# Performance work log

Hardware: AMD Instinct MI355X
Metric: run time of the kernel (lower is better)

The kernel has to match this reference:

```python
import jax, jax.numpy as jnp
import numpy as np

WS = 7        # window size (cubic)
SHIFT = 3     # shift size (cubic)
NH = 6        # num heads
EPS = 1e-5


def _layernorm(x, g, b):
    m = x.mean(-1, keepdims=True)
    v = ((x - m) ** 2).mean(-1, keepdims=True)
    return (x - m) / jnp.sqrt(v + EPS) * g + b


def _win_partition(x, ws):
    # (B,H,W,T,C) -> (B*nW, ws^3, C)
    B, H, W, T, C = x.shape
    x = x.reshape(B, H // ws, ws, W // ws, ws, T // ws, ws, C)
    return x.transpose(0, 1, 3, 5, 2, 4, 6, 7).reshape(-1, ws * ws * ws, C)


def _win_reverse(w, ws, B, H, W, T):
    # (B*nW, ws^3, C) -> (B,H,W,T,C)
    C = w.shape[-1]
    x = w.reshape(B, H // ws, W // ws, T // ws, ws, ws, ws, C)
    return x.transpose(0, 1, 4, 2, 5, 3, 6, 7).reshape(B, H, W, T, C)


def _rel_index(ws):
    # 3D relative position index, (N, N) int, N = ws^3 (torch.meshgrid default 'ij')
    coords = np.stack(np.meshgrid(np.arange(ws), np.arange(ws), np.arange(ws), indexing='ij'))
    cf = coords.reshape(3, -1)
    rel = (cf[:, :, None] - cf[:, None, :]).transpose(1, 2, 0)
    rel[:, :, 0] += ws - 1
    rel[:, :, 1] += ws - 1
    rel[:, :, 2] += ws - 1
    rel[:, :, 0] *= (2 * ws - 1) ** 2
    rel[:, :, 1] *= (2 * ws - 1)
    return rel.sum(-1)


def _compute_mask(Hp, Wp, Tp, ws, shift):
    img = np.zeros((1, Hp, Wp, Tp, 1), np.float32)
    cnt = 0
    sl = (slice(0, -ws), slice(-ws, -shift), slice(-shift, None))
    for h in sl:
        for w in sl:
            for t in sl:
                img[:, h, w, t, :] = cnt
                cnt += 1
    mw = np.asarray(_win_partition(jnp.asarray(img), ws)).reshape(-1, ws ** 3)  # (nW, N)
    am = mw[:, None, :] - mw[:, :, None]
    return jnp.asarray(np.where(am != 0, -100.0, 0.0).astype(np.float32))


def setup_inputs() -> dict:
    key = jax.random.key(0)
    ks = jax.random.split(key, 10)
    B, Hd, Wd, Td, C = 2, 28, 28, 28, 192
    L = Hd * Wd * Td
    Ch = int(C * 4.0)
    s = 0.02
    inp = {
        'x': jax.random.normal(ks[0], (B, L, C), jnp.float32),
        'mask': _compute_mask(Hd, Wd, Td, WS, SHIFT),
        'gamma1': jnp.ones((C,), jnp.float32),
        'beta1': jnp.zeros((C,), jnp.float32),
        'qkv_w': jax.random.normal(ks[1], (3 * C, C), jnp.float32) * s,
        'qkv_b': jnp.zeros((3 * C,), jnp.float32),
        'rpb_table': jax.random.normal(ks[2], ((2 * WS - 1) ** 3, NH), jnp.float32) * s,
        'proj_w': jax.random.normal(ks[3], (C, C), jnp.float32) * s,
        'proj_b': jnp.zeros((C,), jnp.float32),
        'gamma2': jnp.ones((C,), jnp.float32),
        'beta2': jnp.zeros((C,), jnp.float32),
        'fc1_w': jax.random.normal(ks[4], (Ch, C), jnp.float32) * s,
        'fc1_b': jnp.zeros((Ch,), jnp.float32),
        'fc2_w': jax.random.normal(ks[5], (C, Ch), jnp.float32) * s,
        'fc2_b': jnp.zeros((C,), jnp.float32),
        'H': Hd, 'W': Wd, 'T': Td,
    }
    return inp


def reference(x, mask, gamma1, beta1, qkv_w, qkv_b, rpb_table, proj_w, proj_b,
              gamma2, beta2, fc1_w, fc1_b, fc2_w, fc2_b, H, W, T):
    B, L, C = x.shape
    hd = C // NH
    scale = hd ** -0.5
    shortcut = x

    h1 = _layernorm(x, gamma1, beta1).reshape(B, H, W, T, C)
    # H,W,T are multiples of WS -> no padding; cyclic shift for SW-MSA
    shifted = jnp.roll(h1, (-SHIFT, -SHIFT, -SHIFT), axis=(1, 2, 3))
    xw = _win_partition(shifted, WS)            # (B*nW, N, C)
    Bn, N, _ = xw.shape

    qkv = (xw @ qkv_w.T + qkv_b).reshape(Bn, N, 3, NH, hd).transpose(2, 0, 3, 1, 4)
    q, k, v = qkv[0] * scale, qkv[1], qkv[2]     # (Bn, NH, N, hd)
    attn = jnp.einsum('bhnd,bhmd->bhnm', q, k)   # (Bn, NH, N, N)

    idx = _rel_index(WS)
    bias = rpb_table[idx.reshape(-1)].reshape(N, N, NH).transpose(2, 0, 1)
    attn = attn + bias[None]

    nW = mask.shape[0]
    attn = attn.reshape(Bn // nW, nW, NH, N, N) + mask[None, :, None]
    attn = jax.nn.softmax(attn.reshape(Bn, NH, N, N), axis=-1)

    out = jnp.einsum('bhnm,bhmd->bhnd', attn, v).transpose(0, 2, 1, 3).reshape(Bn, N, C)
    out = out @ proj_w.T + proj_b

    shifted = _win_reverse(out, WS, B, H, W, T)
    xr = jnp.roll(shifted, (SHIFT, SHIFT, SHIFT), axis=(1, 2, 3)).reshape(B, L, C)

    x = shortcut + xr
    h2 = _layernorm(x, gamma2, beta2)
    m = jax.nn.gelu(h2 @ fc1_w.T + fc1_b, approximate=False)
    return x + (m @ fc2_w.T + fc2_b)
```

## Files before the change

kernel.cpp:

```cpp
#include <hip/hip_runtime.h>
#include <hip/hip_bf16.h>

typedef unsigned short u16;
typedef unsigned int u32;
typedef __attribute__((ext_vector_type(8))) short s16x8;
typedef __attribute__((ext_vector_type(4))) float f32x4;

__device__ __forceinline__ float bf2f(u16 v) {
    union { u32 u; float f; } x; x.u = ((u32)v) << 16; return x.f;
}
__device__ __forceinline__ u16 f2bf(float f) {
    union { float f; u32 u; } x; x.f = f;
    u32 r = x.u + 0x7fffu + ((x.u >> 16) & 1u);
    return (u16)(r >> 16);
}

#define L_TOK 21952
#define C_DIM 192
#define ATT_SCALE 0.17677669529663687f

__global__ __launch_bounds__(256) void cvt_k(const float* __restrict__ s0,
                                             const float* __restrict__ s1,
                                             const float* __restrict__ s2,
                                             const float* __restrict__ s3,
                                             u16* __restrict__ dst)
{
    int i = blockIdx.x * 256 + threadIdx.x;
    float v;
    if (i < 110592) v = s0[i];
    else if (i < 147456) v = s1[i - 110592];
    else if (i < 294912) v = s2[i - 147456];
    else v = s3[i - 294912];
    dst[i] = f2bf(v);
}

__global__ __launch_bounds__(256) void bias6_k(const float* __restrict__ rpb,
                                               u16* __restrict__ bias6)
{
    const int m = blockIdx.x * 256 + threadIdx.x;
    if (m >= 343) return;
    const int n = blockIdx.y, hh = blockIdx.z;
    int hq = n / 49, r1 = n - hq * 49, wq = r1 / 7, tq = r1 - wq * 7;
    int hm = m / 49, r2 = m - hm * 49, wm = r2 / 7, tm = r2 - wm * 7;
    int idx = ((hq - hm + 6) * 13 + (wq - wm + 6)) * 13 + (tq - tm + 6);
    bias6[((size_t)hh * 343 + n) * 343 + m] = f2bf(rpb[idx * 6 + hh]);
}

template<int MODE>
__global__ __launch_bounds__(256) void ln_k(const float* __restrict__ in,
                                            const float* __restrict__ g,
                                            const float* __restrict__ b,
                                            u16* __restrict__ out)
{
    const int lane = threadIdx.x & 63, wv = threadIdx.x >> 6;
    const int tok = blockIdx.x * 4 + wv;
    size_t base = (size_t)tok * C_DIM;
    float x0 = in[base + lane];
    float x1 = in[base + 64 + lane];
    float x2 = in[base + 128 + lane];
    float s = x0 + x1 + x2;
    float sq = x0 * x0 + x1 * x1 + x2 * x2;
    #pragma unroll
    for (int off = 32; off > 0; off >>= 1) {
        s += __shfl_xor(s, off, 64);
        sq += __shfl_xor(sq, off, 64);
    }
    const float mean = s * (1.0f / 192.0f);
    float var = sq * (1.0f / 192.0f) - mean * mean;
    var = fmaxf(var, 0.0f);
    const float rstd = rsqrtf(var + 1e-5f);

    size_t obase;
    if (MODE == 0) {
        int bi = tok / L_TOK;
        int l = tok - bi * L_TOK;
        int h = l / 784;
        int rm = l - h * 784;
        int w = rm / 28;
        int t = rm - w * 28;
        int hs = h + 25; if (hs >= 28) hs -= 28;
        int ws = w + 25; if (ws >= 28) ws -= 28;
        int ts = t + 25; if (ts >= 28) ts -= 28;
        int win = ((bi * 4 + hs / 7) * 4 + ws / 7) * 4 + ts / 7;
        int n = (hs % 7) * 49 + (ws % 7) * 7 + (ts % 7);
        obase = ((size_t)win * 343 + n) * C_DIM;
    } else {
        obase = base;
    }
    #pragma unroll
    for (int i = 0; i < 3; i++) {
        int c = lane + i * 64;
        float xv = (i == 0) ? x0 : (i == 1) ? x1 : x2;
        float y = (xv - mean) * rstd * g[c] + b[c];
        out[obase + c] = f2bf(y);
    }
}

template<int K, int EPI>
__global__ __launch_bounds__(256) void gemm_k(const u16* __restrict__ A,
                                              const u16* __restrict__ W,
                                              const float* __restrict__ bias,
                                              void* __restrict__ outp,
                                              const void* __restrict__ resp,
                                              int Ncols)
{
    __shared__ __align__(16) u16 As[128 * 32];
    __shared__ __align__(16) u16 Bs[64 * 32];
    const int t = threadIdx.x;
    const int bm = blockIdx.x;
    const int n0 = blockIdx.y * 64;
    const int lane = t & 63, wv = t >> 6;
    const int wm = (wv >> 1) * 64, wn = (wv & 1) * 32;
    const int r16 = lane & 15, quad = lane >> 4;

    f32x4 acc[4][2];
    #pragma unroll
    for (int i = 0; i < 4; i++)
        #pragma unroll
        for (int j = 0; j < 2; j++) acc[i][j] = (f32x4){0.f, 0.f, 0.f, 0.f};

    const int ar = t >> 2, ac = (t & 3) * 8;
    const size_t abase = (size_t)bm * 128 * K;

    for (int k0 = 0; k0 < K; k0 += 32) {
        *(uint4*)&As[ar * 32 + ac] = *(const uint4*)&A[abase + (size_t)ar * K + k0 + ac];
        *(uint4*)&As[(ar + 64) * 32 + ac] = *(const uint4*)&A[abase + (size_t)(ar + 64) * K + k0 + ac];
        *(uint4*)&Bs[ar * 32 + ac] = *(const uint4*)&W[(size_t)(n0 + ar) * K + k0 + ac];
        __syncthreads();
        s16x8 af[4], bf[2];
        #pragma unroll
        for (int fm = 0; fm < 4; fm++)
            af[fm] = *(const s16x8*)&As[(wm + fm * 16 + r16) * 32 + quad * 8];
        #pragma unroll
        for (int fn = 0; fn < 2; fn++)
            bf[fn] = *(const s16x8*)&Bs[(wn + fn * 16 + r16) * 32 + quad * 8];
        #pragma unroll
        for (int fm = 0; fm < 4; fm++)
            #pragma unroll
            for (int fn = 0; fn < 2; fn++)
                acc[fm][fn] = __builtin_amdgcn_mfma_f32_16x16x32_bf16(af[fm], bf[fn], acc[fm][fn], 0, 0, 0);
        __syncthreads();
    }

    #pragma unroll
    for (int fm = 0; fm < 4; fm++) {
        #pragma unroll
        for (int fn = 0; fn < 2; fn++) {
            #pragma unroll
            for (int r = 0; r < 4; r++) {
                const int grow = bm * 128 + wm + fm * 16 + quad * 4 + r;
                const int gcol = n0 + wn + fn * 16 + r16;
                float v = acc[fm][fn][r] + bias[gcol];
                if (EPI == 0) {
                    if (gcol < 192) v *= ATT_SCALE;
                    ((u16*)outp)[(size_t)grow * Ncols + gcol] = f2bf(v);
                } else if (EPI == 1) {
                    v = 0.5f * v * (1.0f + erff(v * 0.70710678118654752f));
                    ((u16*)outp)[(size_t)grow * Ncols + gcol] = f2bf(v);
                } else if (EPI == 2) {
                    size_t o = (size_t)grow * C_DIM + gcol;
                    ((float*)outp)[o] = v + ((const float*)resp)[o];
                } else {
                    int win = grow / 343, n = grow - win * 343;
                    int bi = win >> 6, wi = win & 63;
                    int hw = wi >> 4, ww = (wi >> 2) & 3, tw = wi & 3;
                    int ph = n / 49, rem = n - ph * 49;
                    int pw = rem / 7, pt = rem - pw * 7;
                    int h = hw * 7 + ph + 3; if (h >= 28) h -= 28;
                    int w = ww * 7 + pw + 3; if (w >= 28) w -= 28;
                    int tt = tw * 7 + pt + 3; if (tt >= 28) tt -= 28;
                    int l = (h * 28 + w) * 28 + tt;
                    size_t o = ((size_t)bi * L_TOK + l) * C_DIM + gcol;
                    ((float*)outp)[o] = v + ((const float*)resp)[o];
                }
            }
        }
    }
}

__global__ __launch_bounds__(256, 2) void attn_k(const u16* __restrict__ qkv,
                                                 const u16* __restrict__ bias6,
                                                 u16* __restrict__ out)
{
    __shared__ __align__(16) u16 Ks[352 * 40];
    __shared__ __align__(16) u16 Vt[32 * 360];
    __shared__ __align__(16) u16 Pb[4][16 * 40];
    __shared__ u16 Cn[344];

    const int hh = blockIdx.x;
    const int win = blockIdx.y;
    const int wi = win & 63;
    const int t = threadIdx.x, lane = t & 63, wv = t >> 6;
    const int r16 = lane & 15, quad = lane >> 4;
    const size_t qbase = (size_t)win * 343 * 576 + hh * 32;

    for (int j = t; j < 343 * 4; j += 256) {
        int m = j >> 2, ch = j & 3;
        *(uint4*)&Ks[m * 40 + ch * 8] = *(const uint4*)&qkv[qbase + (size_t)m * 576 + 192 + ch * 8];
    }
    if (t < 36) {
        int m = 343 + (t >> 2), ch = t & 3;
        *(uint4*)&Ks[m * 40 + ch * 8] = (uint4){0u, 0u, 0u, 0u};
    }
    for (int i = t; i < 343 * 16; i += 256) {
        int m = i >> 4, d2 = (i & 15) * 2;
        u32 w2 = *(const u32*)&qkv[qbase + (size_t)m * 576 + 384 + d2];
        Vt[d2 * 360 + m] = (u16)(w2 & 0xffffu);
        Vt[(d2 + 1) * 360 + m] = (u16)(w2 >> 16);
    }
    for (int i = t; i < 32 * 9; i += 256) {
        int d = i / 9, m = 343 + i % 9;
        Vt[d * 360 + m] = 0;
    }
    {
        const int hw = (wi >> 4) & 3, ww = (wi >> 2) & 3, tw = wi & 3;
        for (int n = t; n < 344; n += 256) {
            int nn = n > 342 ? 342 : n;
            int ph = nn / 49, rem = nn - ph * 49;
            int pw = rem / 7, pt = rem - pw * 7;
            int rh = (hw == 3) ? (ph < 4 ? 1 : 2) : 0;
            int rw = (ww == 3) ? (pw < 4 ? 1 : 2) : 0;
            int rt = (tw == 3) ? (pt < 4 ? 1 : 2) : 0;
            Cn[n] = (u16)(rh * 9 + rw * 3 + rt);
        }
    }
    __syncthreads();

    const u16* biash = bias6 + (size_t)hh * 343 * 343;

    u16 cntc[22];
    #pragma unroll
    for (int fn = 0; fn < 22; fn++) {
        int col = fn * 16 + r16; if (col > 342) col = 342;
        cntc[fn] = Cn[col];
    }

    for (int qt = 0; qt < 6; qt++) {
        const int row0 = qt * 64 + wv * 16;
        int qrow = row0 + r16; if (qrow > 342) qrow = 342;
        s16x8 qa = *(const s16x8*)&qkv[qbase + (size_t)qrow * 576 + quad * 8];

        u16 cr[4];
        #pragma unroll
        for (int r = 0; r < 4; r++) {
            int n = row0 + quad * 4 + r; if (n > 342) n = 342;
            cr[r] = Cn[n];
        }

        f32x4 sacc[22];
        #pragma unroll
        for (int fn = 0; fn < 22; fn++) {
            int col = fn * 16 + r16; if (col > 342) col = 342;
            #pragma unroll
            for (int r = 0; r < 4; r++) {
                int n = row0 + quad * 4 + r; if (n > 342) n = 342;
                sacc[fn][r] = bf2f(biash[(size_t)n * 343 + col]);
            }
        }
        #pragma unroll
        for (int fn = 0; fn < 22; fn++) {
            s16x8 kb = *(const s16x8*)&Ks[(fn * 16 + r16) * 40 + quad * 8];
            sacc[fn] = __builtin_amdgcn_mfma_f32_16x16x32_bf16(qa, kb, sacc[fn], 0, 0, 0);
        }

        float rowsum[4] = {0.f, 0.f, 0.f, 0.f};
        #pragma unroll
        for (int fn = 0; fn < 22; fn++) {
            const int col = fn * 16 + r16;
            #pragma unroll
            for (int r = 0; r < 4; r++) {
                float p = 0.0f;
                if (col < 343 && cntc[fn] == cr[r])
                    p = __expf(fminf(sacc[fn][r], 30.0f));
                sacc[fn][r] = p;
                rowsum[r] += p;
            }
        }
        #pragma unroll
        for (int r = 0; r < 4; r++) {
            float v = rowsum[r];
            #pragma unroll
            for (int off = 1; off < 16; off <<= 1) v += __shfl_xor(v, off, 64);
            rowsum[r] = v;
        }

        u16* pw = &Pb[wv][0];
        f32x4 oacc0 = (f32x4){0.f, 0.f, 0.f, 0.f};
        f32x4 oacc1 = (f32x4){0.f, 0.f, 0.f, 0.f};
        #pragma unroll
        for (int c = 0; c < 11; c++) {
            asm volatile("s_waitcnt lgkmcnt(0)" ::: "memory");
            #pragma unroll
            for (int h = 0; h < 2; h++) {
                const int fn = 2 * c + h;
                #pragma unroll
                for (int r = 0; r < 4; r++)
                    pw[(quad * 4 + r) * 40 + h * 16 + r16] = f2bf(sacc[fn][r]);
            }
            asm volatile("s_waitcnt lgkmcnt(0)" ::: "memory");
            s16x8 pa = *(const s16x8*)&pw[r16 * 40 + quad * 8];
            s16x8 vb0 = *(const s16x8*)&Vt[r16 * 360 + c * 32 + quad * 8];
            s16x8 vb1 = *(const s16x8*)&Vt[(16 + r16) * 360 + c * 32 + quad * 8];
            oacc0 = __builtin_amdgcn_mfma_f32_16x16x32_bf16(pa, vb0, oacc0, 0, 0, 0);
            oacc1 = __builtin_amdgcn_mfma_f32_16x16x32_bf16(pa, vb1, oacc1, 0, 0, 0);
        }

        #pragma unroll
        for (int r = 0; r < 4; r++) {
            const int n = row0 + quad * 4 + r;
            if (n < 343) {
                const float rs = rowsum[r];
                const float inv = rs > 0.0f ? 1.0f / rs : 0.0f;
                size_t o = ((size_t)win * 343 + n) * C_DIM + hh * 32;
                out[o + r16] = f2bf(oacc0[r] * inv);
                out[o + 16 + r16] = f2bf(oacc1[r] * inv);
            }
        }
    }
}

extern "C" void kernel_launch(void* const* d_in, const int* in_sizes, int n_in,
                              void* d_out, int out_size, void* d_ws, size_t ws_size,
                              hipStream_t stream)
{
    const float* x      = (const float*)d_in[0];
    const float* g1     = (const float*)d_in[2];
    const float* b1     = (const float*)d_in[3];
    const float* qkv_w  = (const float*)d_in[4];
    const float* qkv_b  = (const float*)d_in[5];
    const float* rpb    = (const float*)d_in[6];
    const float* proj_w = (const float*)d_in[7];
    const float* proj_b = (const float*)d_in[8];
    const float* g2     = (const float*)d_in[9];
    const float* b2     = (const float*)d_in[10];
    const float* fc1_w  = (const float*)d_in[11];
    const float* fc1_b  = (const float*)d_in[12];
    const float* fc2_w  = (const float*)d_in[13];
    const float* fc2_b  = (const float*)d_in[14];

    char* ws = (char*)d_ws;
    u16* xw        = (u16*)(ws + 0);
    u16* bias6     = (u16*)(ws + 0);
    u16* qkv       = (u16*)(ws + 16861184);
    u16* a1        = (u16*)(ws + 0);
    u16* attn_out  = (u16*)(ws + 67444736);
    u16* h2        = attn_out;
    float* x2      = (float*)(ws + 84305920);
    u16* wbf       = (u16*)(ws + 118028288);
    u16* qkv_wb = wbf;
    u16* proj_wb = wbf + 110592;
    u16* fc1_wb = wbf + 147456;
    u16* fc2_wb = wbf + 294912;

    cvt_k<<<dim3(1728), 256, 0, stream>>>(qkv_w, proj_w, fc1_w, fc2_w, wbf);
    ln_k<0><<<dim3(10976), 256, 0, stream>>>(x, g1, b1, xw);
    gemm_k<192, 0><<<dim3(343, 9), 256, 0, stream>>>(xw, qkv_wb, qkv_b, qkv, nullptr, 576);
    bias6_k<<<dim3(2, 343, 6), 256, 0, stream>>>(rpb, bias6);
    attn_k<<<dim3(6, 128), 256, 0, stream>>>(qkv, bias6, attn_out);
    gemm_k<192, 3><<<dim3(343, 3), 256, 0, stream>>>(attn_out, proj_wb, proj_b, x2, x, 192);
    ln_k<1><<<dim3(10976), 256, 0, stream>>>(x2, g2, b2, h2);
    gemm_k<192, 1><<<dim3(343, 12), 256, 0, stream>>>(h2, fc1_wb, fc1_b, a1, nullptr, 768);
    gemm_k<768, 2><<<dim3(343, 3), 256, 0, stream>>>(a1, fc2_wb, fc2_b, d_out, x2, 192);
}
```

Measured before the change: 371.2 us.

## Use direct-to-LDS GEMM loads, exp2 softmax, 512-thread attention, swapped grid order

The GEMM tile loads now go straight from global memory to LDS with global_load_lds instead of passing through registers. The grid is transposed so consecutive blocks share the same A row-tile across N-tiles. The attention kernel moves to 512 threads with 8 waves covering 128 query rows per pass. The softmax switches to exp2 with log2e folded into the q scale and the bias table, P is stored as packed bf16 pairs, and V columns are permuted so each packed P pair matches its V entries. Together these target global-to-LDS latency, L2 reuse, attention occupancy and ALU cost in the softmax, at the price of higher register and LDS pressure per block and a more intricate V layout that must stay matched to P.

```diff
diff --git a/kernel.cpp b/kernel.cpp
--- a/kernel.cpp
+++ b/kernel.cpp
@@ -14,10 +14,20 @@
     u32 r = x.u + 0x7fffu + ((x.u >> 16) & 1u);
     return (u16)(r >> 16);
 }
+__device__ __forceinline__ u32 f2bf_pk(float a, float b) {
+    __hip_bfloat162 hb = __float22bfloat162_rn(make_float2(a, b));
+    union { __hip_bfloat162 h; u32 u; } c; c.h = hb; return c.u;
+}
+__device__ __forceinline__ void gl2lds(const u16* g, u16* l) {
+    __builtin_amdgcn_global_load_lds(
+        (const __attribute__((address_space(1))) unsigned int*)g,
+        (__attribute__((address_space(3))) unsigned int*)l, 16, 0, 0);
+}
 
 #define L_TOK 21952
 #define C_DIM 192
-#define ATT_SCALE 0.17677669529663687f
+#define LOG2E 1.4426950408889634f
+#define Q2SCALE 0.2550565444463649f
 
 __global__ __launch_bounds__(256) void cvt_k(const float* __restrict__ s0,
                                              const float* __restrict__ s1,
@@ -43,7 +53,7 @@
     int hq = n / 49, r1 = n - hq * 49, wq = r1 / 7, tq = r1 - wq * 7;
     int hm = m / 49, r2 = m - hm * 49, wm = r2 / 7, tm = r2 - wm * 7;
     int idx = ((hq - hm + 6) * 13 + (wq - wm + 6)) * 13 + (tq - tm + 6);
-    bias6[((size_t)hh * 343 + n) * 343 + m] = f2bf(rpb[idx * 6 + hh]);
+    bias6[((size_t)hh * 343 + n) * 343 + m] = f2bf(rpb[idx * 6 + hh] * LOG2E);
 }
 
 template<int MODE>
@@ -107,8 +117,8 @@
     __shared__ __align__(16) u16 As[128 * 32];
     __shared__ __align__(16) u16 Bs[64 * 32];
     const int t = threadIdx.x;
-    const int bm = blockIdx.x;
-    const int n0 = blockIdx.y * 64;
+    const int bm = blockIdx.y;
+    const int n0 = blockIdx.x * 64;
     const int lane = t & 63, wv = t >> 6;
     const int wm = (wv >> 1) * 64, wn = (wv & 1) * 32;
     const int r16 = lane & 15, quad = lane >> 4;
@@ -123,9 +133,9 @@
     const size_t abase = (size_t)bm * 128 * K;
 
     for (int k0 = 0; k0 < K; k0 += 32) {
-        *(uint4*)&As[ar * 32 + ac] = *(const uint4*)&A[abase + (size_t)ar * K + k0 + ac];
-        *(uint4*)&As[(ar + 64) * 32 + ac] = *(const uint4*)&A[abase + (size_t)(ar + 64) * K + k0 + ac];
-        *(uint4*)&Bs[ar * 32 + ac] = *(const uint4*)&W[(size_t)(n0 + ar) * K + k0 + ac];
+        gl2lds(&A[abase + (size_t)ar * K + k0 + ac], &As[8 * t]);
+        gl2lds(&A[abase + (size_t)(ar + 64) * K + k0 + ac], &As[2048 + 8 * t]);
+        gl2lds(&W[(size_t)(n0 + ar) * K + k0 + ac], &Bs[8 * t]);
         __syncthreads();
         s16x8 af[4], bf[2];
         #pragma unroll
@@ -152,7 +162,7 @@
                 const int gcol = n0 + wn + fn * 16 + r16;
                 float v = acc[fm][fn][r] + bias[gcol];
                 if (EPI == 0) {
-                    if (gcol < 192) v *= ATT_SCALE;
+                    if (gcol < 192) v *= Q2SCALE;
                     ((u16*)outp)[(size_t)grow * Ncols + gcol] = f2bf(v);
                 } else if (EPI == 1) {
                     v = 0.5f * v * (1.0f + erff(v * 0.70710678118654752f));
@@ -178,13 +188,13 @@
     }
 }
 
-__global__ __launch_bounds__(256, 2) void attn_k(const u16* __restrict__ qkv,
+__global__ __launch_bounds__(512, 4) void attn_k(const u16* __restrict__ qkv,
                                                  const u16* __restrict__ bias6,
                                                  u16* __restrict__ out)
 {
     __shared__ __align__(16) u16 Ks[352 * 40];
     __shared__ __align__(16) u16 Vt[32 * 360];
-    __shared__ __align__(16) u16 Pb[4][16 * 40];
+    __shared__ __align__(16) u16 Pb[8][16 * 40];
     __shared__ u16 Cn[344];
 
     const int hh = blockIdx.x;
@@ -194,7 +204,7 @@
     const int r16 = lane & 15, quad = lane >> 4;
     const size_t qbase = (size_t)win * 343 * 576 + hh * 32;
 
-    for (int j = t; j < 343 * 4; j += 256) {
+    for (int j = t; j < 343 * 4; j += 512) {
         int m = j >> 2, ch = j & 3;
         *(uint4*)&Ks[m * 40 + ch * 8] = *(const uint4*)&qkv[qbase + (size_t)m * 576 + 192 + ch * 8];
     }
@@ -202,19 +212,21 @@
         int m = 343 + (t >> 2), ch = t & 3;
         *(uint4*)&Ks[m * 40 + ch * 8] = (uint4){0u, 0u, 0u, 0u};
     }
-    for (int i = t; i < 343 * 16; i += 256) {
+    for (int i = t; i < 343 * 16; i += 512) {
         int m = i >> 4, d2 = (i & 15) * 2;
+        int pm = (m & ~31) + 2 * (m & 15) + ((m >> 4) & 1);
         u32 w2 = *(const u32*)&qkv[qbase + (size_t)m * 576 + 384 + d2];
-        Vt[d2 * 360 + m] = (u16)(w2 & 0xffffu);
-        Vt[(d2 + 1) * 360 + m] = (u16)(w2 >> 16);
-    }
-    for (int i = t; i < 32 * 9; i += 256) {
+        Vt[d2 * 360 + pm] = (u16)(w2 & 0xffffu);
+        Vt[(d2 + 1) * 360 + pm] = (u16)(w2 >> 16);
+    }
+    for (int i = t; i < 32 * 9; i += 512) {
         int d = i / 9, m = 343 + i % 9;
-        Vt[d * 360 + m] = 0;
+        int pm = (m & ~31) + 2 * (m & 15) + ((m >> 4) & 1);
+        Vt[d * 360 + pm] = 0;
     }
     {
         const int hw = (wi >> 4) & 3, ww = (wi >> 2) & 3, tw = wi & 3;
-        for (int n = t; n < 344; n += 256) {
+        for (int n = t; n < 344; n += 512) {
             int nn = n > 342 ? 342 : n;
             int ph = nn / 49, rem = nn - ph * 49;
             int pw = rem / 7, pt = rem - pw * 7;
@@ -235,8 +247,9 @@
         cntc[fn] = Cn[col];
     }
 
-    for (int qt = 0; qt < 6; qt++) {
-        const int row0 = qt * 64 + wv * 16;
+    for (int qt = 0; qt < 3; qt++) {
+        const int row0 = qt * 128 + wv * 16;
+        if (row0 > 342) continue;
         int qrow = row0 + r16; if (qrow > 342) qrow = 342;
         s16x8 qa = *(const s16x8*)&qkv[qbase + (size_t)qrow * 576 + quad * 8];
 
@@ -271,7 +284,7 @@
             for (int r = 0; r < 4; r++) {
                 float p = 0.0f;
                 if (col < 343 && cntc[fn] == cr[r])
-                    p = __expf(fminf(sacc[fn][r], 30.0f));
+                    p = exp2f(fminf(sacc[fn][r], 42.0f));
                 sacc[fn][r] = p;
                 rowsum[r] += p;
             }
@@ -285,18 +298,15 @@
         }
 
         u16* pw = &Pb[wv][0];
+        u32* pw32 = (u32*)pw;
         f32x4 oacc0 = (f32x4){0.f, 0.f, 0.f, 0.f};
         f32x4 oacc1 = (f32x4){0.f, 0.f, 0.f, 0.f};
         #pragma unroll
         for (int c = 0; c < 11; c++) {
             asm volatile("s_waitcnt lgkmcnt(0)" ::: "memory");
             #pragma unroll
-            for (int h = 0; h < 2; h++) {
-                const int fn = 2 * c + h;
-                #pragma unroll
-                for (int r = 0; r < 4; r++)
-                    pw[(quad * 4 + r) * 40 + h * 16 + r16] = f2bf(sacc[fn][r]);
-            }
+            for (int r = 0; r < 4; r++)
+                pw32[(quad * 4 + r) * 20 + r16] = f2bf_pk(sacc[2 * c][r], sacc[2 * c + 1][r]);
             asm volatile("s_waitcnt lgkmcnt(0)" ::: "memory");
             s16x8 pa = *(const s16x8*)&pw[r16 * 40 + quad * 8];
             s16x8 vb0 = *(const s16x8*)&Vt[r16 * 360 + c * 32 + quad * 8];
@@ -354,11 +364,11 @@
 
     cvt_k<<<dim3(1728), 256, 0, stream>>>(qkv_w, proj_w, fc1_w, fc2_w, wbf);
     ln_k<0><<<dim3(10976), 256, 0, stream>>>(x, g1, b1, xw);
-    gemm_k<192, 0><<<dim3(343, 9), 256, 0, stream>>>(xw, qkv_wb, qkv_b, qkv, nullptr, 576);
+    gemm_k<192, 0><<<dim3(9, 343), 256, 0, stream>>>(xw, qkv_wb, qkv_b, qkv, nullptr, 576);
     bias6_k<<<dim3(2, 343, 6), 256, 0, stream>>>(rpb, bias6);
-    attn_k<<<dim3(6, 128), 256, 0, stream>>>(qkv, bias6, attn_out);
-    gemm_k<192, 3><<<dim3(343, 3), 256, 0, stream>>>(attn_out, proj_wb, proj_b, x2, x, 192);
+    attn_k<<<dim3(6, 128), 512, 0, stream>>>(qkv, bias6, attn_out);
+    gemm_k<192, 3><<<dim3(3, 343), 256, 0, stream>>>(attn_out, proj_wb, proj_b, x2, x, 192);
     ln_k<1><<<dim3(10976), 256, 0, stream>>>(x2, g2, b2, h2);
-    gemm_k<192, 1><<<dim3(343, 12), 256, 0, stream>>>(h2, fc1_wb, fc1_b, a1, nullptr, 768);
-    gemm_k<768, 2><<<dim3(343, 3), 256, 0, stream>>>(a1, fc2_wb, fc2_b, d_out, x2, 192);
-}
+    gemm_k<192, 1><<<dim3(12, 343), 256, 0, stream>>>(h2, fc1_wb, fc1_b, a1, nullptr, 768);
+    gemm_k<768, 2><<<dim3(3, 343), 256, 0, stream>>>(a1, fc2_wb, fc2_b, d_out, x2, 192);
+}
```

Result: slower. 469.7 us (+26.5%).
